# Kernel tuning notes

Hardware: AMD Instinct MI355X
Metric: run time of the kernel (lower is better)

## Reference

```python
import jax, jax.numpy as jnp
import numpy as np

N = 20000   # nodes
E = 320000  # edges (avg degree 16)
K = 3       # Chebyshev order


def _glorot(key, shape):
    fan_in, fan_out = shape[-2], shape[-1]
    lim = (6.0 / (fan_in + fan_out)) ** 0.5
    return jax.random.uniform(key, shape, minval=-lim, maxval=lim, dtype=jnp.float32)


def setup_inputs() -> dict:
    key = jax.random.key(0)
    ks = jax.random.split(key, 8)
    v = jax.random.normal(ks[0], (N, 86), dtype=jnp.float32)
    edges = jax.random.randint(ks[1], (2, E), 0, N, dtype=jnp.int32)
    W1 = _glorot(ks[2], (K, 86, 128));  b1 = jnp.zeros((128,), jnp.float32)
    W2 = _glorot(ks[3], (K, 128, 256)); b2 = jnp.zeros((256,), jnp.float32)
    W3 = _glorot(ks[4], (K, 256, 512)); b3 = jnp.zeros((512,), jnp.float32)
    return {"v": v, "edges": edges, "W1": W1, "b1": b1,
            "W2": W2, "b2": b2, "W3": W3, "b3": b3}


def _cheb_norm(edges, n):
    # PyG ChebConv with sym norm, lambda_max=2: L_hat = L - I = -D^-1/2 A D^-1/2
    # (diagonal entries from get_laplacian (+1) and add_self_loops (-1) cancel).
    # Self loops are removed before computing the Laplacian -> mask them out.
    row, col = edges[0], edges[1]
    w = (row != col).astype(jnp.float32)
    deg = jax.ops.segment_sum(w, row, num_segments=n)
    dinv = jnp.where(deg > 0, jax.lax.rsqrt(jnp.maximum(deg, 1e-12)), 0.0)
    norm_w = -dinv[row] * w * dinv[col]  # [E]
    return row, col, norm_w


def _cheb_conv(x, row, col, norm_w, W, b):
    # W: [K, in, out]
    def prop(z):  # L_hat @ z via edge gather + segment scatter-add
        return jax.ops.segment_sum(norm_w[:, None] * z[col], row, num_segments=x.shape[0])
    Tx0 = x
    out = Tx0 @ W[0]
    Tx1 = prop(Tx0)
    out = out + Tx1 @ W[1]
    Tx2 = 2.0 * prop(Tx1) - Tx0
    out = out + Tx2 @ W[2]
    return out + b


def reference(v, edges, W1, b1, W2, b2, W3, b3):
    row, col, norm_w = _cheb_norm(edges, v.shape[0])
    nk = jax.random.key(42)
    x1 = jax.nn.relu(_cheb_conv(v, row, col, norm_w, W1, b1))
    x1 = x1 * jax.random.normal(jax.random.fold_in(nk, 1), x1.shape, x1.dtype)
    x2 = jax.nn.relu(_cheb_conv(x1, row, col, norm_w, W2, b2))
    x2 = x2 * jax.random.normal(jax.random.fold_in(nk, 2), x2.shape, x2.dtype)
    x3 = jax.nn.relu(_cheb_conv(x2, row, col, norm_w, W3, b3))
    x3 = x3 * jax.random.normal(jax.random.fold_in(nk, 3), x3.shape, x3.dtype)
    return (x1, x2, x3)
```

## Files before the change

### kernel.cpp

```cpp
#include <hip/hip_runtime.h>
#include <stdint.h>
#include <math.h>

#define DEV static __device__ __forceinline__

typedef __attribute__((ext_vector_type(8))) short bf16x8;
typedef __attribute__((ext_vector_type(4))) float f32x4;
typedef __attribute__((ext_vector_type(8))) unsigned short u16x8;

DEV uint32_t rotl32(uint32_t v, int d) { return (v << d) | (v >> (32 - d)); }

DEV void threefry2x32(uint32_t k0, uint32_t k1, uint32_t& x0, uint32_t& x1) {
  const uint32_t k2 = k0 ^ k1 ^ 0x1BD11BDAu;
  x0 += k0; x1 += k1;
#define TFR(R) { x0 += x1; x1 = rotl32(x1, R) ^ x0; }
  TFR(13) TFR(15) TFR(26) TFR(6)
  x0 += k1; x1 += k2 + 1u;
  TFR(17) TFR(29) TFR(16) TFR(24)
  x0 += k2; x1 += k0 + 2u;
  TFR(13) TFR(15) TFR(26) TFR(6)
  x0 += k0; x1 += k1 + 3u;
  TFR(17) TFR(29) TFR(16) TFR(24)
  x0 += k1; x1 += k2 + 4u;
  TFR(13) TFR(15) TFR(26) TFR(6)
  x0 += k2; x1 += k0 + 5u;
#undef TFR
}

DEV float erfinv_f32(float x) {
  float w = -log1pf(-x * x);
  float p;
  if (w < 5.0f) {
    w -= 2.5f;
    p = 2.81022636e-08f;
    p = fmaf(p, w, 3.43273939e-07f);
    p = fmaf(p, w, -3.5233877e-06f);
    p = fmaf(p, w, -4.39150654e-06f);
    p = fmaf(p, w, 0.00021858087f);
    p = fmaf(p, w, -0.00125372503f);
    p = fmaf(p, w, -0.00417768164f);
    p = fmaf(p, w, 0.246640727f);
    p = fmaf(p, w, 1.50140941f);
  } else {
    w = sqrtf(w) - 3.0f;
    p = -0.000200214257f;
    p = fmaf(p, w, 0.000100950558f);
    p = fmaf(p, w, 0.00134934322f);
    p = fmaf(p, w, -0.00367342844f);
    p = fmaf(p, w, 0.00573950773f);
    p = fmaf(p, w, -0.0076224613f);
    p = fmaf(p, w, 0.00943887047f);
    p = fmaf(p, w, 1.00167406f);
    p = fmaf(p, w, 2.83297682f);
  }
  return p * x;
}

DEV float normal_from_bits(uint32_t bits) {
  float f = __uint_as_float((bits >> 9) | 0x3F800000u) - 1.0f;
  const float lo = -0.99999994f;
  float u = fmaf(f, 2.0f, lo);
  u = fmaxf(u, lo);
  return 1.41421356f * erfinv_f32(u);
}

DEV unsigned short f2bf(float f) {
  uint32_t u = __float_as_uint(f);
  uint32_t r = u + 0x7FFFu + ((u >> 16) & 1u);
  return (unsigned short)(r >> 16);
}

DEV float bf2f(uint32_t h) { return __uint_as_float(h << 16); }

__global__ void count_kernel(const int* __restrict__ rows, const int* __restrict__ cols,
                             int* __restrict__ counts, int* __restrict__ degs, int E) {
  int e = blockIdx.x * blockDim.x + threadIdx.x;
  if (e < E) {
    int r = rows[e];
    atomicAdd(&counts[r], 1);
    if (r != cols[e]) atomicAdd(&degs[r], 1);
  }
}

__global__ void dinv_kernel(const int* __restrict__ degs, float* __restrict__ dinv, int N) {
  int i = blockIdx.x * blockDim.x + threadIdx.x;
  if (i < N) {
    int d = degs[i];
    dinv[i] = d > 0 ? rsqrtf((float)d) : 0.0f;
  }
}

#define SCAN_T 1024
__global__ __launch_bounds__(SCAN_T) void scan_kernel(const int* __restrict__ counts,
                                                      int* __restrict__ row_ptr,
                                                      int* __restrict__ cursor, int N) {
  __shared__ int sa[SCAN_T], sb[SCAN_T];
  const int t = threadIdx.x;
  const int CH = (N + SCAN_T - 1) / SCAN_T;
  int base = t * CH;
  int psum = 0;
  for (int k = 0; k < CH; ++k) {
    int idx = base + k;
    if (idx < N) psum += counts[idx];
  }
  sa[t] = psum;
  __syncthreads();
  int* src = sa; int* dst = sb;
  for (int off = 1; off < SCAN_T; off <<= 1) {
    int v = src[t];
    if (t >= off) v += src[t - off];
    dst[t] = v;
    __syncthreads();
    int* tmp = src; src = dst; dst = tmp;
  }
  int running = src[t] - psum;
  for (int k = 0; k < CH; ++k) {
    int idx = base + k;
    if (idx < N) {
      row_ptr[idx] = running;
      cursor[idx] = running;
      running += counts[idx];
    }
  }
  if (t == SCAN_T - 1) row_ptr[N] = running;
}

__global__ void fill_kernel(const int* __restrict__ rows, const int* __restrict__ cols,
                            const float* __restrict__ dinv, int* __restrict__ cursor,
                            float2* __restrict__ ecv, int E) {
  int e = blockIdx.x * blockDim.x + threadIdx.x;
  if (e < E) {
    int r = rows[e], c = cols[e];
    float w = (r != c) ? -dinv[r] * dinv[c] : 0.0f;
    int pos = atomicAdd(&cursor[r], 1);
    ecv[pos] = make_float2(__int_as_float(c), w);
  }
}

template <int VEC, int BSRC>
DEV void ldrow(const void* base, size_t off, float* v) {
  if (BSRC) {
    const unsigned short* p = (const unsigned short*)base + off;
    if (VEC == 4) {
      uint2 u = *(const uint2*)p;
      v[0] = bf2f(u.x & 0xffffu); v[1] = bf2f(u.x >> 16);
      v[2] = bf2f(u.y & 0xffffu); v[3] = bf2f(u.y >> 16);
    } else {
      uint32_t u = *(const uint32_t*)p;
      v[0] = bf2f(u & 0xffffu); v[1] = bf2f(u >> 16);
    }
  } else {
    const float* p = (const float*)base + off;
    if (VEC == 4) {
      float4 t = *(const float4*)p;
      v[0] = t.x; v[1] = t.y; v[2] = t.z; v[3] = t.w;
    } else {
      float2 t = *(const float2*)p;
      v[0] = t.x; v[1] = t.y;
    }
  }
}

template <int VEC, int SUB, int BSRC>
__global__ __launch_bounds__(256) void gather_prop(
    const int* __restrict__ row_ptr, const float2* __restrict__ ecv,
    const void* __restrict__ xsrc, int sstride,
    const float* __restrict__ xsub, int substride,
    unsigned short* __restrict__ outb, int N, int F, int Fpad) {
  const int wave = threadIdx.x >> 6, lane = threadIdx.x & 63;
  const int node = blockIdx.x * 4 + wave;
  if (node >= N) return;
  const int f0 = lane * VEC;
  if (f0 >= Fpad) return;
  const bool live = (f0 + VEC) <= F;
  float acc[VEC] = {};
  if (live) {
    const int s = row_ptr[node], e = row_ptr[node + 1];
    int j = s;
    for (; j + 4 <= e; j += 4) {
      float2 c0 = ecv[j], c1 = ecv[j + 1], c2 = ecv[j + 2], c3 = ecv[j + 3];
      float v0[VEC], v1[VEC], v2[VEC], v3[VEC];
      ldrow<VEC, BSRC>(xsrc, (size_t)__float_as_int(c0.x) * sstride + f0, v0);
      ldrow<VEC, BSRC>(xsrc, (size_t)__float_as_int(c1.x) * sstride + f0, v1);
      ldrow<VEC, BSRC>(xsrc, (size_t)__float_as_int(c2.x) * sstride + f0, v2);
      ldrow<VEC, BSRC>(xsrc, (size_t)__float_as_int(c3.x) * sstride + f0, v3);
#pragma unroll
      for (int q = 0; q < VEC; ++q) {
        acc[q] = fmaf(c0.y, v0[q], acc[q]);
        acc[q] = fmaf(c1.y, v1[q], acc[q]);
        acc[q] = fmaf(c2.y, v2[q], acc[q]);
        acc[q] = fmaf(c3.y, v3[q], acc[q]);
      }
    }
    for (; j < e; ++j) {
      float2 cw = ecv[j];
      float vv[VEC];
      ldrow<VEC, BSRC>(xsrc, (size_t)__float_as_int(cw.x) * sstride + f0, vv);
#pragma unroll
      for (int q = 0; q < VEC; ++q) acc[q] = fmaf(cw.y, vv[q], acc[q]);
    }
    if (SUB) {
      const float* sb = xsub + (size_t)node * substride + f0;
#pragma unroll
      for (int q = 0; q < VEC; ++q) acc[q] = fmaf(2.0f, acc[q], -sb[q]);
    }
  }
  size_t ob = (size_t)node * Fpad + f0;
  if (VEC == 4) {
    uint2 u;
    u.x = (uint32_t)f2bf(acc[0]) | ((uint32_t)f2bf(acc[1]) << 16);
    u.y = (uint32_t)f2bf(acc[2]) | ((uint32_t)f2bf(acc[3]) << 16);
    *(uint2*)&outb[ob] = u;
  } else {
    uint32_t u = (uint32_t)f2bf(acc[0]) | ((uint32_t)f2bf(acc[1]) << 16);
    *(uint32_t*)&outb[ob] = u;
  }
}

__global__ void wtrans_kernel(const float* __restrict__ W, unsigned short* __restrict__ Wt,
                              int F, int Fpad, int O) {
  int idx = blockIdx.x * 256 + threadIdx.x;
  int total = 3 * O * Fpad;
  if (idx >= total) return;
  int k = idx % Fpad;
  int o = (idx / Fpad) % O;
  int p = idx / (Fpad * O);
  Wt[idx] = (k < F) ? f2bf(W[((size_t)p * F + k) * O + o]) : (unsigned short)0;
}

__global__ void vconv_kernel(const float* __restrict__ v, unsigned short* __restrict__ vb, int N) {
  int i = blockIdx.x * 256 + threadIdx.x;
  if (i >= N * 96) return;
  int r = i / 96, k = i % 96;
  vb[i] = (k < 86) ? f2bf(v[(size_t)r * 86 + k]) : (unsigned short)0;
}

template <int BM, int FPAD, int KS>
__global__ __launch_bounds__(512, 4) void gemm3_lds(
    const unsigned short* __restrict__ A0, const unsigned short* __restrict__ A1,
    const unsigned short* __restrict__ A2,
    const unsigned short* __restrict__ Wt, const float* __restrict__ bias,
    int M, int O, float* __restrict__ out, unsigned short* __restrict__ outb,
    int obstride, int fold) {
  constexpr int BN = 128;
  constexpr int CPR = KS / 8;
  constexpr int LST = KS + 8;
  constexpr int NA = BM * CPR;
  constexpr int NB = BN * CPR;
  constexpr int ACH = (NA + 511) / 512;
  constexpr int BCH = (NB + 511) / 512;
  constexpr int MFR = BM / 32;
  constexpr int KK = KS / 32;

  __shared__ unsigned short sA[BM * LST];
  __shared__ unsigned short sB[BN * LST];

  const int tid = threadIdx.x;
  const int lane = tid & 63;
  const int wave = tid >> 6;
  const int wm = wave >> 2, wo = wave & 3;
  const int bm = blockIdx.x * BM;
  const int bo = blockIdx.y * BN;
  const int l15 = lane & 15;
  const int kg = (lane >> 4) * 8;

  f32x4 acc[MFR][2] = {};
  const unsigned short* As[3] = {A0, A1, A2};

#pragma unroll
  for (int p = 0; p < 3; ++p) {
    const unsigned short* __restrict__ A = As[p];
    const unsigned short* __restrict__ B = Wt + (size_t)p * O * FPAD;
    for (int k0 = 0; k0 < FPAD; k0 += KS) {
      u16x8 ra[ACH], rb[BCH];
#pragma unroll
      for (int c = 0; c < ACH; ++c) {
        int idx = tid + c * 512;
        if (NA % 512 == 0 || idx < NA) {
          int row = idx / CPR, ch = (idx % CPR) * 8;
          int gm = bm + row; if (gm >= M) gm = M - 1;
          ra[c] = *(const u16x8*)(A + (size_t)gm * FPAD + k0 + ch);
        }
      }
#pragma unroll
      for (int c = 0; c < BCH; ++c) {
        int idx = tid + c * 512;
        if (NB % 512 == 0 || idx < NB) {
          int row = idx / CPR, ch = (idx % CPR) * 8;
          rb[c] = *(const u16x8*)(B + (size_t)(bo + row) * FPAD + k0 + ch);
        }
      }
      __syncthreads();
#pragma unroll
      for (int c = 0; c < ACH; ++c) {
        int idx = tid + c * 512;
        if (NA % 512 == 0 || idx < NA) {
          int row = idx / CPR, ch = (idx % CPR) * 8;
          *(u16x8*)&sA[row * LST + ch] = ra[c];
        }
      }
#pragma unroll
      for (int c = 0; c < BCH; ++c) {
        int idx = tid + c * 512;
        if (NB % 512 == 0 || idx < NB) {
          int row = idx / CPR, ch = (idx % CPR) * 8;
          *(u16x8*)&sB[row * LST + ch] = rb[c];
        }
      }
      __syncthreads();
#pragma unroll
      for (int kk = 0; kk < KK; ++kk) {
        bf16x8 af[MFR], bfr[2];
#pragma unroll
        for (int mi = 0; mi < MFR; ++mi)
          af[mi] = *(const bf16x8*)&sA[(wm * (BM / 2) + mi * 16 + l15) * LST + kk * 32 + kg];
#pragma unroll
        for (int ni = 0; ni < 2; ++ni)
          bfr[ni] = *(const bf16x8*)&sB[(wo * 32 + ni * 16 + l15) * LST + kk * 32 + kg];
#pragma unroll
        for (int mi = 0; mi < MFR; ++mi)
#pragma unroll
          for (int ni = 0; ni < 2; ++ni)
            acc[mi][ni] = __builtin_amdgcn_mfma_f32_16x16x32_bf16(af[mi], bfr[ni], acc[mi][ni], 0, 0, 0);
      }
    }
  }

  uint32_t f0 = 0u, f1 = (uint32_t)fold;
  threefry2x32(0u, 42u, f0, f1);
  const int r0 = (lane >> 4) * 4;
#pragma unroll
  for (int mi = 0; mi < MFR; ++mi) {
#pragma unroll
    for (int r = 0; r < 4; ++r) {
      int gm = bm + wm * (BM / 2) + mi * 16 + r0 + r;
      if (gm >= M) continue;
#pragma unroll
      for (int ni = 0; ni < 2; ++ni) {
        int go = bo + wo * 32 + ni * 16 + l15;
        float vv = acc[mi][ni][r] + bias[go];
        vv = vv > 0.0f ? vv : 0.0f;
        uint32_t a = 0u, b = (uint32_t)(gm * O + go);
        threefry2x32(f0, f1, a, b);
        float res = vv * normal_from_bits(a ^ b);
        out[(size_t)gm * O + go] = res;
        if (outb) outb[(size_t)gm * obstride + go] = f2bf(res);
      }
    }
  }
}

extern "C" void kernel_launch(void* const* d_in, const int* in_sizes, int n_in,
                              void* d_out, int out_size, void* d_ws, size_t ws_size,
                              hipStream_t stream) {
  const float* v    = (const float*)d_in[0];
  const int*  edges = (const int*)d_in[1];
  const float* W1 = (const float*)d_in[2];
  const float* b1 = (const float*)d_in[3];
  const float* W2 = (const float*)d_in[4];
  const float* b2 = (const float*)d_in[5];
  const float* W3 = (const float*)d_in[6];
  const float* b3 = (const float*)d_in[7];
  float* out = (float*)d_out;

  const int N = in_sizes[0] / 86;
  const int E = in_sizes[1] / 2;
  const int* rows = edges;
  const int* cols = edges + E;

  uintptr_t cur = (uintptr_t)d_ws;
  auto alloc = [&](size_t bytes) {
    cur = (cur + 15) & ~(uintptr_t)15;
    void* p = (void*)cur;
    cur += bytes;
    return p;
  };
  float2* ecv          = (float2*)alloc((size_t)E * 8);
  int* counts          = (int*)alloc((size_t)N * 4);
  int* degs            = (int*)alloc((size_t)N * 4);
  int* row_ptr         = (int*)alloc((size_t)(N + 1) * 4);
  int* cursor          = (int*)alloc((size_t)N * 4);
  float* dinv          = (float*)alloc((size_t)N * 4);
  unsigned short* tx1b = (unsigned short*)alloc((size_t)N * 256 * 2);
  unsigned short* tx2b = (unsigned short*)alloc((size_t)N * 256 * 2);
  unsigned short* vb   = (unsigned short*)alloc((size_t)N * 96 * 2);
  unsigned short* x1b  = (unsigned short*)alloc((size_t)N * 128 * 2);
  unsigned short* x2b  = (unsigned short*)alloc((size_t)N * 256 * 2);
  unsigned short* Wt   = (unsigned short*)alloc((size_t)3 * 512 * 256 * 2);

  float* x1 = out;
  float* x2 = x1 + (size_t)N * 128;
  float* x3 = x2 + (size_t)N * 256;

  hipMemsetAsync(counts, 0, (size_t)2 * N * sizeof(int), stream);
  count_kernel<<<(E + 255) / 256, 256, 0, stream>>>(rows, cols, counts, degs, E);
  dinv_kernel<<<(N + 255) / 256, 256, 0, stream>>>(degs, dinv, N);
  scan_kernel<<<1, SCAN_T, 0, stream>>>(counts, row_ptr, cursor, N);
  fill_kernel<<<(E + 255) / 256, 256, 0, stream>>>(rows, cols, dinv, cursor, ecv, E);
  vconv_kernel<<<(N * 96 + 255) / 256, 256, 0, stream>>>(v, vb, N);

  const int pblocks = (N + 3) / 4;

  {
    wtrans_kernel<<<(3 * 128 * 96 + 255) / 256, 256, 0, stream>>>(W1, Wt, 86, 96, 128);
    gather_prop<2, 0, 1><<<pblocks, 256, 0, stream>>>(row_ptr, ecv, vb, 96, nullptr, 0, tx1b, N, 86, 96);
    gather_prop<2, 1, 1><<<pblocks, 256, 0, stream>>>(row_ptr, ecv, tx1b, 96, v, 86, tx2b, N, 86, 96);
    dim3 g((N + 63) / 64, 1);
    gemm3_lds<64, 96, 32><<<g, 512, 0, stream>>>(vb, tx1b, tx2b, Wt, b1, N, 128, x1, x1b, 128, 1);
  }
  {
    wtrans_kernel<<<(3 * 256 * 128 + 255) / 256, 256, 0, stream>>>(W2, Wt, 128, 128, 256);
    gather_prop<2, 0, 1><<<pblocks, 256, 0, stream>>>(row_ptr, ecv, x1b, 128, nullptr, 0, tx1b, N, 128, 128);
    gather_prop<2, 1, 1><<<pblocks, 256, 0, stream>>>(row_ptr, ecv, tx1b, 128, x1, 128, tx2b, N, 128, 128);
    dim3 g((N + 127) / 128, 2);
    gemm3_lds<128, 128, 64><<<g, 512, 0, stream>>>(x1b, tx1b, tx2b, Wt, b2, N, 256, x2, x2b, 256, 2);
  }
  {
    wtrans_kernel<<<(3 * 512 * 256 + 255) / 256, 256, 0, stream>>>(W3, Wt, 256, 256, 512);
    gather_prop<4, 0, 1><<<pblocks, 256, 0, stream>>>(row_ptr, ecv, x2b, 256, nullptr, 0, tx1b, N, 256, 256);
    gather_prop<4, 1, 1><<<pblocks, 256, 0, stream>>>(row_ptr, ecv, tx1b, 256, x2, 256, tx2b, N, 256, 256);
    dim3 g((N + 127) / 128, 4);
    gemm3_lds<128, 256, 64><<<g, 512, 0, stream>>>(x2b, tx1b, tx2b, Wt, b3, N, 512, x3, nullptr, 0, 3);
  }
}
```

Measured before the change: 401.9 us.

## Double-buffer LDS in fused Chebyshev GEMM and unroll gather by eight edges

The GEMM kernel now uses two LDS buffers. It prefetches the next K-slice from global memory into registers while MFMAs run on the current slice, which cuts one barrier per step and hides global load latency. The gather kernel unrolls its edge loop from 4 to 8 to keep more independent row loads in flight, and the unused fp32 source path is removed. The cost is twice the LDS and more live registers, which could lower occupancy under the 512-thread launch bound.

```diff
diff --git a/kernel.cpp b/kernel.cpp
--- a/kernel.cpp
+++ b/kernel.cpp
@@ -137,34 +137,23 @@
   }
 }
 
-template <int VEC, int BSRC>
-DEV void ldrow(const void* base, size_t off, float* v) {
-  if (BSRC) {
-    const unsigned short* p = (const unsigned short*)base + off;
-    if (VEC == 4) {
-      uint2 u = *(const uint2*)p;
-      v[0] = bf2f(u.x & 0xffffu); v[1] = bf2f(u.x >> 16);
-      v[2] = bf2f(u.y & 0xffffu); v[3] = bf2f(u.y >> 16);
-    } else {
-      uint32_t u = *(const uint32_t*)p;
-      v[0] = bf2f(u & 0xffffu); v[1] = bf2f(u >> 16);
-    }
+template <int VEC>
+DEV void ldrow(const unsigned short* base, size_t off, float* v) {
+  const unsigned short* p = base + off;
+  if (VEC == 4) {
+    uint2 u = *(const uint2*)p;
+    v[0] = bf2f(u.x & 0xffffu); v[1] = bf2f(u.x >> 16);
+    v[2] = bf2f(u.y & 0xffffu); v[3] = bf2f(u.y >> 16);
   } else {
-    const float* p = (const float*)base + off;
-    if (VEC == 4) {
-      float4 t = *(const float4*)p;
-      v[0] = t.x; v[1] = t.y; v[2] = t.z; v[3] = t.w;
-    } else {
-      float2 t = *(const float2*)p;
-      v[0] = t.x; v[1] = t.y;
-    }
-  }
-}
-
-template <int VEC, int SUB, int BSRC>
+    uint32_t u = *(const uint32_t*)p;
+    v[0] = bf2f(u & 0xffffu); v[1] = bf2f(u >> 16);
+  }
+}
+
+template <int VEC, int SUB>
 __global__ __launch_bounds__(256) void gather_prop(
     const int* __restrict__ row_ptr, const float2* __restrict__ ecv,
-    const void* __restrict__ xsrc, int sstride,
+    const unsigned short* __restrict__ xsrc, int sstride,
     const float* __restrict__ xsub, int substride,
     unsigned short* __restrict__ outb, int N, int F, int Fpad) {
   const int wave = threadIdx.x >> 6, lane = threadIdx.x & 63;
@@ -177,32 +166,30 @@
   if (live) {
     const int s = row_ptr[node], e = row_ptr[node + 1];
     int j = s;
-    for (; j + 4 <= e; j += 4) {
-      float2 c0 = ecv[j], c1 = ecv[j + 1], c2 = ecv[j + 2], c3 = ecv[j + 3];
-      float v0[VEC], v1[VEC], v2[VEC], v3[VEC];
-      ldrow<VEC, BSRC>(xsrc, (size_t)__float_as_int(c0.x) * sstride + f0, v0);
-      ldrow<VEC, BSRC>(xsrc, (size_t)__float_as_int(c1.x) * sstride + f0, v1);
-      ldrow<VEC, BSRC>(xsrc, (size_t)__float_as_int(c2.x) * sstride + f0, v2);
-      ldrow<VEC, BSRC>(xsrc, (size_t)__float_as_int(c3.x) * sstride + f0, v3);
-#pragma unroll
-      for (int q = 0; q < VEC; ++q) {
-        acc[q] = fmaf(c0.y, v0[q], acc[q]);
-        acc[q] = fmaf(c1.y, v1[q], acc[q]);
-        acc[q] = fmaf(c2.y, v2[q], acc[q]);
-        acc[q] = fmaf(c3.y, v3[q], acc[q]);
-      }
+    for (; j + 8 <= e; j += 8) {
+      float2 cw[8];
+      float vv[8][VEC];
+#pragma unroll
+      for (int q = 0; q < 8; ++q) cw[q] = ecv[j + q];
+#pragma unroll
+      for (int q = 0; q < 8; ++q)
+        ldrow<VEC>(xsrc, (size_t)__float_as_int(cw[q].x) * sstride + f0, vv[q]);
+#pragma unroll
+      for (int q = 0; q < 8; ++q)
+#pragma unroll
+        for (int z = 0; z < VEC; ++z) acc[z] = fmaf(cw[q].y, vv[q][z], acc[z]);
     }
     for (; j < e; ++j) {
       float2 cw = ecv[j];
       float vv[VEC];
-      ldrow<VEC, BSRC>(xsrc, (size_t)__float_as_int(cw.x) * sstride + f0, vv);
-#pragma unroll
-      for (int q = 0; q < VEC; ++q) acc[q] = fmaf(cw.y, vv[q], acc[q]);
+      ldrow<VEC>(xsrc, (size_t)__float_as_int(cw.x) * sstride + f0, vv);
+#pragma unroll
+      for (int z = 0; z < VEC; ++z) acc[z] = fmaf(cw.y, vv[z], acc[z]);
     }
     if (SUB) {
       const float* sb = xsub + (size_t)node * substride + f0;
 #pragma unroll
-      for (int q = 0; q < VEC; ++q) acc[q] = fmaf(2.0f, acc[q], -sb[q]);
+      for (int z = 0; z < VEC; ++z) acc[z] = fmaf(2.0f, acc[z], -sb[z]);
     }
   }
   size_t ob = (size_t)node * Fpad + f0;
@@ -236,13 +223,15 @@
 }
 
 template <int BM, int FPAD, int KS>
-__global__ __launch_bounds__(512, 4) void gemm3_lds(
+__global__ __launch_bounds__(512, 4) void gemm3_db(
     const unsigned short* __restrict__ A0, const unsigned short* __restrict__ A1,
     const unsigned short* __restrict__ A2,
     const unsigned short* __restrict__ Wt, const float* __restrict__ bias,
     int M, int O, float* __restrict__ out, unsigned short* __restrict__ outb,
     int obstride, int fold) {
   constexpr int BN = 128;
+  constexpr int NSP = FPAD / KS;
+  constexpr int NSTEP = 3 * NSP;
   constexpr int CPR = KS / 8;
   constexpr int LST = KS + 8;
   constexpr int NA = BM * CPR;
@@ -252,8 +241,8 @@
   constexpr int MFR = BM / 32;
   constexpr int KK = KS / 32;
 
-  __shared__ unsigned short sA[BM * LST];
-  __shared__ unsigned short sB[BN * LST];
+  __shared__ unsigned short sA[2][BM * LST];
+  __shared__ unsigned short sB[2][BN * LST];
 
   const int tid = threadIdx.x;
   const int lane = tid & 63;
@@ -267,62 +256,81 @@
   f32x4 acc[MFR][2] = {};
   const unsigned short* As[3] = {A0, A1, A2};
 
-#pragma unroll
-  for (int p = 0; p < 3; ++p) {
+  u16x8 ra[ACH], rb[BCH];
+
+  auto issue = [&](int s) {
+    int p = s / NSP, k0 = (s % NSP) * KS;
     const unsigned short* __restrict__ A = As[p];
     const unsigned short* __restrict__ B = Wt + (size_t)p * O * FPAD;
-    for (int k0 = 0; k0 < FPAD; k0 += KS) {
-      u16x8 ra[ACH], rb[BCH];
-#pragma unroll
-      for (int c = 0; c < ACH; ++c) {
-        int idx = tid + c * 512;
-        if (NA % 512 == 0 || idx < NA) {
-          int row = idx / CPR, ch = (idx % CPR) * 8;
-          int gm = bm + row; if (gm >= M) gm = M - 1;
-          ra[c] = *(const u16x8*)(A + (size_t)gm * FPAD + k0 + ch);
-        }
+#pragma unroll
+    for (int c = 0; c < ACH; ++c) {
+      int idx = tid + c * 512;
+      if (NA % 512 == 0 || idx < NA) {
+        int row = idx / CPR, ch = (idx % CPR) * 8;
+        int gm = bm + row; if (gm >= M) gm = M - 1;
+        ra[c] = *(const u16x8*)(A + (size_t)gm * FPAD + k0 + ch);
       }
-#pragma unroll
-      for (int c = 0; c < BCH; ++c) {
-        int idx = tid + c * 512;
-        if (NB % 512 == 0 || idx < NB) {
-          int row = idx / CPR, ch = (idx % CPR) * 8;
-          rb[c] = *(const u16x8*)(B + (size_t)(bo + row) * FPAD + k0 + ch);
-        }
+    }
+#pragma unroll
+    for (int c = 0; c < BCH; ++c) {
+      int idx = tid + c * 512;
+      if (NB % 512 == 0 || idx < NB) {
+        int row = idx / CPR, ch = (idx % CPR) * 8;
+        rb[c] = *(const u16x8*)(B + (size_t)(bo + row) * FPAD + k0 + ch);
       }
+    }
+  };
+
+  auto lds_write = [&](int buf) {
+#pragma unroll
+    for (int c = 0; c < ACH; ++c) {
+      int idx = tid + c * 512;
+      if (NA % 512 == 0 || idx < NA) {
+        int row = idx / CPR, ch = (idx % CPR) * 8;
+        *(u16x8*)&sA[buf][row * LST + ch] = ra[c];
+      }
+    }
+#pragma unroll
+    for (int c = 0; c < BCH; ++c) {
+      int idx = tid + c * 512;
+      if (NB % 512 == 0 || idx < NB) {
+        int row = idx / CPR, ch = (idx % CPR) * 8;
+        *(u16x8*)&sB[buf][row * LST + ch] = rb[c];
+      }
+    }
+  };
+
+  auto compute = [&](int buf) {
+#pragma unroll
+    for (int kk = 0; kk < KK; ++kk) {
+      bf16x8 af[MFR], bfr[2];
+#pragma unroll
+      for (int mi = 0; mi < MFR; ++mi)
+        af[mi] = *(const bf16x8*)&sA[buf][(wm * (BM / 2) + mi * 16 + l15) * LST + kk * 32 + kg];
+#pragma unroll
+      for (int ni = 0; ni < 2; ++ni)
+        bfr[ni] = *(const bf16x8*)&sB[buf][(wo * 32 + ni * 16 + l15) * LST + kk * 32 + kg];
+#pragma unroll
+      for (int mi = 0; mi < MFR; ++mi)
+#pragma unroll
+        for (int ni = 0; ni < 2; ++ni)
+          acc[mi][ni] = __builtin_amdgcn_mfma_f32_16x16x32_bf16(af[mi], bfr[ni], acc[mi][ni], 0, 0, 0);
+    }
+  };
+
+  issue(0);
+  lds_write(0);
+  __syncthreads();
+
+  int cur = 0;
+#pragma unroll
+  for (int s = 0; s < NSTEP; ++s) {
+    if (s + 1 < NSTEP) issue(s + 1);
+    compute(cur);
+    if (s + 1 < NSTEP) {
+      lds_write(cur ^ 1);
       __syncthreads();
-#pragma unroll
-      for (int c = 0; c < ACH; ++c) {
-        int idx = tid + c * 512;
-        if (NA % 512 == 0 || idx < NA) {
-          int row = idx / CPR, ch = (idx % CPR) * 8;
-          *(u16x8*)&sA[row * LST + ch] = ra[c];
-        }
-      }
-#pragma unroll
-      for (int c = 0; c < BCH; ++c) {
-        int idx = tid + c * 512;
-        if (NB % 512 == 0 || idx < NB) {
-          int row = idx / CPR, ch = (idx % CPR) * 8;
-          *(u16x8*)&sB[row * LST + ch] = rb[c];
-        }
-      }
-      __syncthreads();
-#pragma unroll
-      for (int kk = 0; kk < KK; ++kk) {
-        bf16x8 af[MFR], bfr[2];
-#pragma unroll
-        for (int mi = 0; mi < MFR; ++mi)
-          af[mi] = *(const bf16x8*)&sA[(wm * (BM / 2) + mi * 16 + l15) * LST + kk * 32 + kg];
-#pragma unroll
-        for (int ni = 0; ni < 2; ++ni)
-          bfr[ni] = *(const bf16x8*)&sB[(wo * 32 + ni * 16 + l15) * LST + kk * 32 + kg];
-#pragma unroll
-        for (int mi = 0; mi < MFR; ++mi)
-#pragma unroll
-          for (int ni = 0; ni < 2; ++ni)
-            acc[mi][ni] = __builtin_amdgcn_mfma_f32_16x16x32_bf16(af[mi], bfr[ni], acc[mi][ni], 0, 0, 0);
-      }
+      cur ^= 1;
     }
   }
 
@@ -403,23 +411,23 @@
 
   {
     wtrans_kernel<<<(3 * 128 * 96 + 255) / 256, 256, 0, stream>>>(W1, Wt, 86, 96, 128);
-    gather_prop<2, 0, 1><<<pblocks, 256, 0, stream>>>(row_ptr, ecv, vb, 96, nullptr, 0, tx1b, N, 86, 96);
-    gather_prop<2, 1, 1><<<pblocks, 256, 0, stream>>>(row_ptr, ecv, tx1b, 96, v, 86, tx2b, N, 86, 96);
+    gather_prop<2, 0><<<pblocks, 256, 0, stream>>>(row_ptr, ecv, vb, 96, nullptr, 0, tx1b, N, 86, 96);
+    gather_prop<2, 1><<<pblocks, 256, 0, stream>>>(row_ptr, ecv, tx1b, 96, v, 86, tx2b, N, 86, 96);
     dim3 g((N + 63) / 64, 1);
-    gemm3_lds<64, 96, 32><<<g, 512, 0, stream>>>(vb, tx1b, tx2b, Wt, b1, N, 128, x1, x1b, 128, 1);
+    gemm3_db<64, 96, 32><<<g, 512, 0, stream>>>(vb, tx1b, tx2b, Wt, b1, N, 128, x1, x1b, 128, 1);
   }
   {
     wtrans_kernel<<<(3 * 256 * 128 + 255) / 256, 256, 0, stream>>>(W2, Wt, 128, 128, 256);
-    gather_prop<2, 0, 1><<<pblocks, 256, 0, stream>>>(row_ptr, ecv, x1b, 128, nullptr, 0, tx1b, N, 128, 128);
-    gather_prop<2, 1, 1><<<pblocks, 256, 0, stream>>>(row_ptr, ecv, tx1b, 128, x1, 128, tx2b, N, 128, 128);
+    gather_prop<2, 0><<<pblocks, 256, 0, stream>>>(row_ptr, ecv, x1b, 128, nullptr, 0, tx1b, N, 128, 128);
+    gather_prop<2, 1><<<pblocks, 256, 0, stream>>>(row_ptr, ecv, tx1b, 128, x1, 128, tx2b, N, 128, 128);
     dim3 g((N + 127) / 128, 2);
-    gemm3_lds<128, 128, 64><<<g, 512, 0, stream>>>(x1b, tx1b, tx2b, Wt, b2, N, 256, x2, x2b, 256, 2);
+    gemm3_db<128, 128, 64><<<g, 512, 0, stream>>>(x1b, tx1b, tx2b, Wt, b2, N, 256, x2, x2b, 256, 2);
   }
   {
     wtrans_kernel<<<(3 * 512 * 256 + 255) / 256, 256, 0, stream>>>(W3, Wt, 256, 256, 512);
-    gather_prop<4, 0, 1><<<pblocks, 256, 0, stream>>>(row_ptr, ecv, x2b, 256, nullptr, 0, tx1b, N, 256, 256);
-    gather_prop<4, 1, 1><<<pblocks, 256, 0, stream>>>(row_ptr, ecv, tx1b, 256, x2, 256, tx2b, N, 256, 256);
+    gather_prop<4, 0><<<pblocks, 256, 0, stream>>>(row_ptr, ecv, x2b, 256, nullptr, 0, tx1b, N, 256, 256);
+    gather_prop<4, 1><<<pblocks, 256, 0, stream>>>(row_ptr, ecv, tx1b, 256, x2, 256, tx2b, N, 256, 256);
     dim3 g((N + 127) / 128, 4);
-    gemm3_lds<128, 256, 64><<<g, 512, 0, stream>>>(x2b, tx1b, tx2b, Wt, b3, N, 512, x3, nullptr, 0, 3);
-  }
-}
+    gemm3_db<128, 256, 64><<<g, 512, 0, stream>>>(x2b, tx1b, tx2b, Wt, b3, N, 512, x3, nullptr, 0, 3);
+  }
+}
```

After: 408.0 us. Within noise of the previous version (+1.5%).
